# Optimization experiments

Hardware: AMD Instinct MI355X
Metric: run time of the kernel (lower is better)

Reference implementation:

```python
import jax, jax.numpy as jnp
import numpy as np

N, D, M, K = 65536, 128, 4096, 64

def _xavier_uniform(key, shape):
    fan_out, fan_in = shape
    limit = float(np.sqrt(6.0 / (fan_in + fan_out)))
    return jax.random.uniform(key, shape, jnp.float32, -limit, limit)

def setup_inputs() -> dict:
    key = jax.random.key(0)
    kx, ke, kd = jax.random.split(key, 3)
    x = jax.random.normal(kx, (N, D), jnp.float32)
    W_enc = _xavier_uniform(ke, (M, D))          # [n_latents, input_dim]
    W_dec = _xavier_uniform(kd, (D, M))          # [input_dim, n_latents]
    # normalize decoder columns to unit norm (dim=0), clamped at 1e-8
    norms = jnp.maximum(jnp.linalg.norm(W_dec, axis=0, keepdims=True), 1e-8)
    W_dec = W_dec / norms
    b_enc = jnp.zeros((M,), jnp.float32)
    b_dec = jnp.zeros((D,), jnp.float32)
    return {"x": x, "W_enc": W_enc, "b_enc": b_enc, "W_dec": W_dec, "b_dec": b_dec}

def reference(x, W_enc, b_enc, W_dec, b_dec):
    # encode: z_pre = relu(W_enc @ (x - b_dec) + b_enc)
    z_pre = jax.nn.relu((x - b_dec) @ W_enc.T + b_enc)          # [N, M]
    # TopK activation: keep k largest, zero the rest
    vals, idx = jax.lax.top_k(z_pre, K)                          # [N, K]
    rows = jnp.arange(z_pre.shape[0])[:, None]
    z = jnp.zeros_like(z_pre).at[rows, idx].set(vals)            # sparse [N, M]
    # decode: x_hat = z @ W_dec.T + b_dec
    x_hat = z @ W_dec.T + b_dec                                  # [N, D]
    return (x_hat, z)
```

## Files before the change

### kernel.cpp

```cpp
#include <hip/hip_runtime.h>
#include <cstdint>

#define DDIM 128
#define MLAT 4096
#define KSEL 64

typedef __bf16 bf16x8 __attribute__((ext_vector_type(8)));
typedef float  f32x4  __attribute__((ext_vector_type(4)));

__device__ __forceinline__ ushort bf16rn(float v) {
    unsigned b = __float_as_uint(v);
    return (ushort)((b + 0x7FFFu + ((b >> 16) & 1u)) >> 16);
}

__global__ __launch_bounds__(256) void k_prep(
        const float* __restrict__ x, const float* __restrict__ bdec,
        ushort* __restrict__ xhi, ushort* __restrict__ xlo,
        const float* __restrict__ Wenc,
        ushort* __restrict__ whiP, ushort* __restrict__ wloP,
        const float* __restrict__ Wdec, float* __restrict__ WdT) {
    int b = blockIdx.x;
    if (b < 8192) {
        int e = (b * 256 + threadIdx.x) * 4;
        float4 v = *(const float4*)(x + e);
        float4 bd = *(const float4*)(bdec + (e & 127));
        float a[4] = {v.x - bd.x, v.y - bd.y, v.z - bd.z, v.w - bd.w};
        ushort4 h, l;
        ushort* hp = (ushort*)&h; ushort* lp = (ushort*)&l;
#pragma unroll
        for (int i = 0; i < 4; ++i) {
            unsigned ua = __float_as_uint(a[i]);
            unsigned rh = (ua + 0x7FFFu + ((ua >> 16) & 1u)) & 0xFFFF0000u;
            float lo = a[i] - __uint_as_float(rh);
            hp[i] = (ushort)(rh >> 16);
            lp[i] = bf16rn(lo);
        }
        *(ushort4*)(xhi + e) = h;
        *(ushort4*)(xlo + e) = l;
    } else if (b < 8704) {
        int e = ((b - 8192) * 256 + threadIdx.x) * 4;
        float4 v = *(const float4*)(Wenc + e);
        float a[4] = {v.x, v.y, v.z, v.w};
        int c = e >> 7, k0 = e & 127;
        int ks = k0 >> 5, lq = (k0 >> 3) & 3, j0 = k0 & 7;
        int out = (((c >> 4) * 4 + ks) * 4 + lq) * 128 + (c & 15) * 8 + j0;
        ushort4 h, l;
        ushort* hp = (ushort*)&h; ushort* lp = (ushort*)&l;
#pragma unroll
        for (int i = 0; i < 4; ++i) {
            unsigned ua = __float_as_uint(a[i]);
            unsigned rh = (ua + 0x7FFFu + ((ua >> 16) & 1u)) & 0xFFFF0000u;
            float lo = a[i] - __uint_as_float(rh);
            hp[i] = (ushort)(rh >> 16);
            lp[i] = bf16rn(lo);
        }
        *(ushort4*)(whiP + out) = h;
        *(ushort4*)(wloP + out) = l;
    } else {
        int tid = (b - 8704) * 256 + threadIdx.x;
        int d = tid >> 12, j = tid & 4095;
        WdT[j * DDIM + d] = Wdec[tid];
    }
}

__global__ __launch_bounds__(256, 2) void k_encode_mfma(
        const ushort* __restrict__ xhi, const ushort* __restrict__ xlo,
        const ushort* __restrict__ whiP, const ushort* __restrict__ wloP,
        const float* __restrict__ benc, float* __restrict__ zout) {
    __shared__ __attribute__((aligned(16))) ushort Ah[128 * 128];
    __shared__ __attribute__((aligned(16))) ushort Al[128 * 128];

    const int t    = threadIdx.x;
    const int lane = t & 63;
    const int w    = t >> 6;
    const int i0   = blockIdx.x << 7;

    {
        int row = t >> 1, half = t & 1;
        const ushort* sh = xhi + (size_t)(i0 + row) * DDIM + half * 64;
        const ushort* sl = xlo + (size_t)(i0 + row) * DDIM + half * 64;
        int base = row * 256 + half * 128;
        int swz  = (row & 7) << 4;
#pragma unroll
        for (int j = 0; j < 8; ++j) {
            int off = (base + j * 16) ^ swz;
            *(bf16x8*)((char*)Ah + off) = *(const bf16x8*)(sh + j * 8);
            *(bf16x8*)((char*)Al + off) = *(const bf16x8*)(sl + j * 8);
        }
    }
    __syncthreads();

    const int lr = lane & 15;
    const int lq = lane >> 4;

    for (int cp = 0; cp < 16; ++cp) {
        const int jb = cp * 256 + (w << 6);
        const int tb = jb >> 4;
        f32x4 acc[8][4];
#pragma unroll
        for (int rf = 0; rf < 8; ++rf)
#pragma unroll
            for (int cf = 0; cf < 4; ++cf) acc[rf][cf] = (f32x4){0.f, 0.f, 0.f, 0.f};

#define BOFF(cf, ks) ((size_t)((((tb + (cf)) << 2) + (ks)) << 9) + (lane << 3))
        bf16x8 bhc[4], blc[4];
#pragma unroll
        for (int cf = 0; cf < 4; ++cf) {
            bhc[cf] = *(const bf16x8*)(whiP + BOFF(cf, 0));
            blc[cf] = *(const bf16x8*)(wloP + BOFF(cf, 0));
        }
#pragma unroll
        for (int ks = 0; ks < 4; ++ks) {
            bf16x8 bhn[4], bln[4];
            if (ks < 3) {
#pragma unroll
                for (int cf = 0; cf < 4; ++cf) {
                    bhn[cf] = *(const bf16x8*)(whiP + BOFF(cf, ks + 1));
                    bln[cf] = *(const bf16x8*)(wloP + BOFF(cf, ks + 1));
                }
            }
#pragma unroll
            for (int rf = 0; rf < 8; ++rf) {
                int row = rf * 16 + lr;
                int off = (row * 256 + ks * 64 + lq * 16) ^ ((row & 7) << 4);
                bf16x8 ah = *(const bf16x8*)((const char*)Ah + off);
                bf16x8 al = *(const bf16x8*)((const char*)Al + off);
#pragma unroll
                for (int cf = 0; cf < 4; ++cf) {
                    acc[rf][cf] = __builtin_amdgcn_mfma_f32_16x16x32_bf16(ah, bhc[cf], acc[rf][cf], 0, 0, 0);
                    acc[rf][cf] = __builtin_amdgcn_mfma_f32_16x16x32_bf16(ah, blc[cf], acc[rf][cf], 0, 0, 0);
                    acc[rf][cf] = __builtin_amdgcn_mfma_f32_16x16x32_bf16(al, bhc[cf], acc[rf][cf], 0, 0, 0);
                }
            }
            if (ks < 3) {
#pragma unroll
                for (int cf = 0; cf < 4; ++cf) { bhc[cf] = bhn[cf]; blc[cf] = bln[cf]; }
            }
        }
#undef BOFF
#pragma unroll
        for (int rf = 0; rf < 8; ++rf)
#pragma unroll
            for (int cf = 0; cf < 4; ++cf) {
                int col = jb + cf * 16 + lr;
                float be = benc[col];
#pragma unroll
                for (int r = 0; r < 4; ++r) {
                    int row = i0 + rf * 16 + lq * 4 + r;
                    zout[(size_t)row * MLAT + col] = fmaxf(acc[rf][cf][r] + be, 0.f);
                }
            }
    }
}

__global__ __launch_bounds__(128, 8) void k_topk_decode(
        float* __restrict__ zbuf, float* __restrict__ xhat,
        const float* __restrict__ WdT, const float* __restrict__ bdec,
        const float* __restrict__ x, const float* __restrict__ Wenc,
        const float* __restrict__ benc) {
    __shared__ float sval[KSEL];
    __shared__ int   sidx[KSEL];
    __shared__ float bval[128];
    __shared__ int   bidx[128];
    __shared__ unsigned char bselm[128];
    __shared__ unsigned scom[4];
    __shared__ int stot[2];

    const int tid  = threadIdx.x;
    const int lane = tid & 63;
    const int w    = tid >> 6;
    const size_t row = blockIdx.x;
    float* zr = zbuf + row * MLAT;
    const uint4* zu = (const uint4*)zr + (w << 9);

    uint4 u[8];
#pragma unroll
    for (int q = 0; q < 8; ++q) u[q] = zu[(q << 6) + lane];

    unsigned mx = 0u;
#pragma unroll
    for (int q = 0; q < 8; ++q)
        mx = max(mx, max(max(u[q].x, u[q].y), max(u[q].z, u[q].w)));
#pragma unroll
    for (int d = 32; d >= 1; d >>= 1) mx = max(mx, (unsigned)__shfl_xor((int)mx, d, 64));
    if (lane == 0) scom[w] = mx;
    __syncthreads();
    mx = max(scom[0], scom[1]);
    __syncthreads();

#define CNT_GE(T, OUTC)                                              \
    {                                                                \
        int _c = 0;                                                  \
        _Pragma("unroll")                                            \
        for (int q = 0; q < 8; ++q) {                                \
            _c += __popcll(__ballot(u[q].x >= (T)));                 \
            _c += __popcll(__ballot(u[q].y >= (T)));                 \
            _c += __popcll(__ballot(u[q].z >= (T)));                 \
            _c += __popcll(__ballot(u[q].w >= (T)));                 \
        }                                                            \
        if (lane == 0) scom[2 + w] = (unsigned)_c;                   \
        __syncthreads();                                             \
        OUTC = (int)(scom[2] + scom[3]);                             \
        __syncthreads();                                             \
    }

    unsigned T;
    {
        unsigned hi = mx + 1u;
        unsigned lo = (mx > 0x01800000u) ? (mx - 0x01800000u) : 0u;
        int c;
        CNT_GE(lo, c);
        if (c < KSEL) { lo = 0u; c = MLAT; }
        if (c == KSEL) {
            T = lo;
        } else {
            for (;;) {
                if (hi - lo <= 1u) { T = lo; break; }
                unsigned mid = lo + ((hi - lo) >> 1);
                int cm;
                CNT_GE(mid, cm);
                if (cm == KSEL) { T = mid; break; }
                if (cm > KSEL) lo = mid; else hi = mid;
            }
        }
    }

    const float tau   = __uint_as_float(T);
    const float DELTA = 2.5e-4f;
    const float PAD   = 5.0e-5f;
    const unsigned DH = __float_as_uint(tau + DELTA + PAD);
    const unsigned DL = __float_as_uint(fmaxf(tau - DELTA, 0.f));

    unsigned inm = 0u, bandm = 0u;
#pragma unroll
    for (int q = 0; q < 8; ++q) {
        unsigned vv[4] = {u[q].x, u[q].y, u[q].z, u[q].w};
#pragma unroll
        for (int c = 0; c < 4; ++c) {
            unsigned bit = 1u << (4 * q + c);
            if (vv[c] > DH) inm |= bit;
            else if (vv[c] >= DL) bandm |= bit;
        }
    }
    {
        int packed = (__popc(inm) << 16) | __popc(bandm);
#pragma unroll
        for (int d = 32; d >= 1; d >>= 1) packed += __shfl_xor(packed, d, 64);
        if (lane == 0) scom[2 + w] = (unsigned)packed;
        __syncthreads();
    }
    int A   = (int)((scom[2] >> 16) + (scom[3] >> 16));
    int BCt = (int)((scom[2] & 0xFFFFu) + (scom[3] & 0xFFFFu));
    __syncthreads();
    int need = KSEL - A;

    unsigned sel;
    if (need <= 0) {
        sel = inm;
    } else if (BCt == need) {
        sel = inm | bandm;
    } else {
        int BC2 = min(BCt, 128);
        int bc = __popc(bandm);
        int pre = bc;
#pragma unroll
        for (int d = 1; d < 64; d <<= 1) {
            int y = __shfl_up(pre, d, 64);
            if (lane >= d) pre += y;
        }
        int wtot = __shfl(pre, 63, 64);
        if (lane == 0) stot[w] = wtot;
        __syncthreads();
        int sbase = (pre - bc) + (w ? stot[0] : 0);
        {
            unsigned mm = bandm; int o = 0;
            while (mm) {
                int bp = __ffs(mm) - 1; mm &= mm - 1;
                int slot = sbase + o; ++o;
                if (slot < 128)
                    bidx[slot] = (w << 11) + ((bp >> 2) << 8) + (lane << 2) + (bp & 3);
            }
        }
        __syncthreads();
        for (int s = tid; s < BC2; s += 128) {
            int j = bidx[s];
            const float* wr = Wenc + (size_t)j * DDIM;
            const float* xr = x + row * DDIM;
            float a = 0.f;
            for (int k = 0; k < DDIM; ++k) a = fmaf(xr[k] - bdec[k], wr[k], a);
            bval[s] = fmaxf(a + benc[j], 0.f);
        }
        __syncthreads();
        if (tid == 0) {
            for (int s = 0; s < BC2; ++s) bselm[s] = 0;
            int take = min(need, BC2);
            for (int it = 0; it < take; ++it) {
                float bv = -1.f; int bi = 0x7FFFFFFF, bs = 0;
                for (int s = 0; s < BC2; ++s) {
                    if (bselm[s]) continue;
                    float v = bval[s]; int j = bidx[s];
                    if (v > bv || (v == bv && j < bi)) { bv = v; bi = j; bs = s; }
                }
                bselm[bs] = 1;
            }
        }
        __syncthreads();
        sel = inm;
        {
            unsigned mm = bandm; int o = 0;
            while (mm) {
                int bp = __ffs(mm) - 1; mm &= mm - 1;
                int slot = sbase + o; ++o;
                if (slot < 128 && bselm[slot]) sel |= 1u << bp;
            }
        }
        __syncthreads();
    }

    int scnt = __popc(sel);
    int pre = scnt;
#pragma unroll
    for (int d = 1; d < 64; d <<= 1) {
        int y = __shfl_up(pre, d, 64);
        if (lane >= d) pre += y;
    }
    int wtot2 = __shfl(pre, 63, 64);
    if (lane == 0) stot[w] = wtot2;
    __syncthreads();
    int pos = pre - scnt + (w ? stot[0] : 0);
    int total = stot[0] + stot[1];

    uint4* zw = (uint4*)zr + (w << 9);
#pragma unroll
    for (int q = 0; q < 8; ++q) {
        uint4 o;
        bool s0 = (sel >> (4 * q + 0)) & 1u;
        bool s1 = (sel >> (4 * q + 1)) & 1u;
        bool s2 = (sel >> (4 * q + 2)) & 1u;
        bool s3 = (sel >> (4 * q + 3)) & 1u;
        o.x = s0 ? u[q].x : 0u;
        o.y = s1 ? u[q].y : 0u;
        o.z = s2 ? u[q].z : 0u;
        o.w = s3 ? u[q].w : 0u;
        int base = (w << 11) + (q << 8) + (lane << 2);
        if (s0 && pos < KSEL) { sval[pos] = __uint_as_float(u[q].x); sidx[pos] = base + 0; ++pos; }
        if (s1 && pos < KSEL) { sval[pos] = __uint_as_float(u[q].y); sidx[pos] = base + 1; ++pos; }
        if (s2 && pos < KSEL) { sval[pos] = __uint_as_float(u[q].z); sidx[pos] = base + 2; ++pos; }
        if (s3 && pos < KSEL) { sval[pos] = __uint_as_float(u[q].w); sidx[pos] = base + 3; ++pos; }
        zw[(q << 6) + lane] = o;
    }
    __syncthreads();

    float a = bdec[tid];
    int tt = min(total, KSEL);
#pragma unroll 4
    for (int s = 0; s < tt; ++s) {
        float v = sval[s];
        int   j = sidx[s];
        a = fmaf(v, WdT[(size_t)j * DDIM + tid], a);
    }
    xhat[row * DDIM + tid] = a;
}

extern "C" void kernel_launch(void* const* d_in, const int* in_sizes, int n_in,
                              void* d_out, int out_size, void* d_ws, size_t ws_size,
                              hipStream_t stream) {
    const float* x    = (const float*)d_in[0];
    const float* Wenc = (const float*)d_in[1];
    const float* benc = (const float*)d_in[2];
    const float* Wdec = (const float*)d_in[3];
    const float* bdec = (const float*)d_in[4];

    const int N = in_sizes[0] / DDIM;
    float* xhat = (float*)d_out;
    float* zbuf = (float*)d_out + (size_t)N * DDIM;

    ushort* xhi = (ushort*)d_out;
    ushort* xlo = xhi + (size_t)N * DDIM;

    ushort* whiP = (ushort*)d_ws;
    ushort* wloP = whiP + (size_t)MLAT * DDIM;
    float*  WdT  = (float*)((char*)d_ws + 2u * 1024u * 1024u);

    k_prep<<<dim3(8192 + 512 + 2048), dim3(256), 0, stream>>>(
        x, bdec, xhi, xlo, Wenc, whiP, wloP, Wdec, WdT);
    k_encode_mfma<<<dim3(N / 128), dim3(256), 0, stream>>>(
        xhi, xlo, whiP, wloP, benc, zbuf);
    k_topk_decode<<<dim3(N), dim3(128), 0, stream>>>(
        zbuf, xhat, WdT, bdec, x, Wenc, benc);
}
```

Baseline: 842.8 us.

## Fuse x bf16 split into encode kernel, add nontemporal stores, drop barriers

Moves the x minus b_dec hi/lo bf16 split from the prep kernel into the encode kernel's shared-memory load. This removes the write and reread of the 64 MB xhi/xlo buffers. The z and x_hat stores and the z loads now use nontemporal builtins. Count reductions in the top-k kernel use double-buffered shared slots so one barrier per step can be dropped. The extra conversion work inside encode adds a little latency before the MFMA loop starts.

```diff
diff --git a/kernel.cpp b/kernel.cpp
--- a/kernel.cpp
+++ b/kernel.cpp
@@ -5,8 +5,10 @@
 #define MLAT 4096
 #define KSEL 64
 
-typedef __bf16 bf16x8 __attribute__((ext_vector_type(8)));
-typedef float  f32x4  __attribute__((ext_vector_type(4)));
+typedef __bf16  bf16x8  __attribute__((ext_vector_type(8)));
+typedef float   f32x4   __attribute__((ext_vector_type(4)));
+typedef ushort  ushort8 __attribute__((ext_vector_type(8)));
+typedef unsigned uint32x4 __attribute__((ext_vector_type(4)));
 
 __device__ __forceinline__ ushort bf16rn(float v) {
     unsigned b = __float_as_uint(v);
@@ -14,31 +16,12 @@
 }
 
 __global__ __launch_bounds__(256) void k_prep(
-        const float* __restrict__ x, const float* __restrict__ bdec,
-        ushort* __restrict__ xhi, ushort* __restrict__ xlo,
         const float* __restrict__ Wenc,
         ushort* __restrict__ whiP, ushort* __restrict__ wloP,
         const float* __restrict__ Wdec, float* __restrict__ WdT) {
     int b = blockIdx.x;
-    if (b < 8192) {
+    if (b < 512) {
         int e = (b * 256 + threadIdx.x) * 4;
-        float4 v = *(const float4*)(x + e);
-        float4 bd = *(const float4*)(bdec + (e & 127));
-        float a[4] = {v.x - bd.x, v.y - bd.y, v.z - bd.z, v.w - bd.w};
-        ushort4 h, l;
-        ushort* hp = (ushort*)&h; ushort* lp = (ushort*)&l;
-#pragma unroll
-        for (int i = 0; i < 4; ++i) {
-            unsigned ua = __float_as_uint(a[i]);
-            unsigned rh = (ua + 0x7FFFu + ((ua >> 16) & 1u)) & 0xFFFF0000u;
-            float lo = a[i] - __uint_as_float(rh);
-            hp[i] = (ushort)(rh >> 16);
-            lp[i] = bf16rn(lo);
-        }
-        *(ushort4*)(xhi + e) = h;
-        *(ushort4*)(xlo + e) = l;
-    } else if (b < 8704) {
-        int e = ((b - 8192) * 256 + threadIdx.x) * 4;
         float4 v = *(const float4*)(Wenc + e);
         float a[4] = {v.x, v.y, v.z, v.w};
         int c = e >> 7, k0 = e & 127;
@@ -57,14 +40,14 @@
         *(ushort4*)(whiP + out) = h;
         *(ushort4*)(wloP + out) = l;
     } else {
-        int tid = (b - 8704) * 256 + threadIdx.x;
+        int tid = (b - 512) * 256 + threadIdx.x;
         int d = tid >> 12, j = tid & 4095;
         WdT[j * DDIM + d] = Wdec[tid];
     }
 }
 
 __global__ __launch_bounds__(256, 2) void k_encode_mfma(
-        const ushort* __restrict__ xhi, const ushort* __restrict__ xlo,
+        const float* __restrict__ x, const float* __restrict__ bdec,
         const ushort* __restrict__ whiP, const ushort* __restrict__ wloP,
         const float* __restrict__ benc, float* __restrict__ zout) {
     __shared__ __attribute__((aligned(16))) ushort Ah[128 * 128];
@@ -77,15 +60,30 @@
 
     {
         int row = t >> 1, half = t & 1;
-        const ushort* sh = xhi + (size_t)(i0 + row) * DDIM + half * 64;
-        const ushort* sl = xlo + (size_t)(i0 + row) * DDIM + half * 64;
+        const float* xr = x + (size_t)(i0 + row) * DDIM + half * 64;
+        const float* bd = bdec + half * 64;
         int base = row * 256 + half * 128;
         int swz  = (row & 7) << 4;
 #pragma unroll
         for (int j = 0; j < 8; ++j) {
+            float4 v0 = *(const float4*)(xr + j * 8);
+            float4 v1 = *(const float4*)(xr + j * 8 + 4);
+            float4 b0 = *(const float4*)(bd + j * 8);
+            float4 b1 = *(const float4*)(bd + j * 8 + 4);
+            float a[8] = {v0.x - b0.x, v0.y - b0.y, v0.z - b0.z, v0.w - b0.w,
+                          v1.x - b1.x, v1.y - b1.y, v1.z - b1.z, v1.w - b1.w};
+            ushort8 h8, l8;
+#pragma unroll
+            for (int i = 0; i < 8; ++i) {
+                unsigned ua = __float_as_uint(a[i]);
+                unsigned rh = (ua + 0x7FFFu + ((ua >> 16) & 1u)) & 0xFFFF0000u;
+                float lo = a[i] - __uint_as_float(rh);
+                h8[i] = (ushort)(rh >> 16);
+                l8[i] = bf16rn(lo);
+            }
             int off = (base + j * 16) ^ swz;
-            *(bf16x8*)((char*)Ah + off) = *(const bf16x8*)(sh + j * 8);
-            *(bf16x8*)((char*)Al + off) = *(const bf16x8*)(sl + j * 8);
+            *(ushort8*)((char*)Ah + off) = h8;
+            *(ushort8*)((char*)Al + off) = l8;
         }
     }
     __syncthreads();
@@ -147,7 +145,8 @@
 #pragma unroll
                 for (int r = 0; r < 4; ++r) {
                     int row = i0 + rf * 16 + lq * 4 + r;
-                    zout[(size_t)row * MLAT + col] = fmaxf(acc[rf][cf][r] + be, 0.f);
+                    __builtin_nontemporal_store(fmaxf(acc[rf][cf][r] + be, 0.f),
+                                                &zout[(size_t)row * MLAT + col]);
                 }
             }
     }
@@ -163,7 +162,7 @@
     __shared__ float bval[128];
     __shared__ int   bidx[128];
     __shared__ unsigned char bselm[128];
-    __shared__ unsigned scom[4];
+    __shared__ unsigned scom[6];
     __shared__ int stot[2];
 
     const int tid  = threadIdx.x;
@@ -171,37 +170,37 @@
     const int w    = tid >> 6;
     const size_t row = blockIdx.x;
     float* zr = zbuf + row * MLAT;
-    const uint4* zu = (const uint4*)zr + (w << 9);
-
-    uint4 u[8];
-#pragma unroll
-    for (int q = 0; q < 8; ++q) u[q] = zu[(q << 6) + lane];
+    const uint32x4* zu = (const uint32x4*)zr + (w << 9);
+
+    uint32x4 u[8];
+#pragma unroll
+    for (int q = 0; q < 8; ++q) u[q] = __builtin_nontemporal_load(zu + (q << 6) + lane);
 
     unsigned mx = 0u;
 #pragma unroll
     for (int q = 0; q < 8; ++q)
-        mx = max(mx, max(max(u[q].x, u[q].y), max(u[q].z, u[q].w)));
+        mx = max(mx, max(max(u[q][0], u[q][1]), max(u[q][2], u[q][3])));
 #pragma unroll
     for (int d = 32; d >= 1; d >>= 1) mx = max(mx, (unsigned)__shfl_xor((int)mx, d, 64));
     if (lane == 0) scom[w] = mx;
     __syncthreads();
     mx = max(scom[0], scom[1]);
-    __syncthreads();
-
+
+    unsigned par = 0;
 #define CNT_GE(T, OUTC)                                              \
     {                                                                \
         int _c = 0;                                                  \
         _Pragma("unroll")                                            \
         for (int q = 0; q < 8; ++q) {                                \
-            _c += __popcll(__ballot(u[q].x >= (T)));                 \
-            _c += __popcll(__ballot(u[q].y >= (T)));                 \
-            _c += __popcll(__ballot(u[q].z >= (T)));                 \
-            _c += __popcll(__ballot(u[q].w >= (T)));                 \
+            _c += __popcll(__ballot(u[q][0] >= (T)));                \
+            _c += __popcll(__ballot(u[q][1] >= (T)));                \
+            _c += __popcll(__ballot(u[q][2] >= (T)));                \
+            _c += __popcll(__ballot(u[q][3] >= (T)));                \
         }                                                            \
-        if (lane == 0) scom[2 + w] = (unsigned)_c;                   \
+        if (lane == 0) scom[2 + 2 * par + w] = (unsigned)_c;         \
         __syncthreads();                                             \
-        OUTC = (int)(scom[2] + scom[3]);                             \
-        __syncthreads();                                             \
+        OUTC = (int)(scom[2 + 2 * par] + scom[3 + 2 * par]);         \
+        par ^= 1u;                                                   \
     }
 
     unsigned T;
@@ -234,24 +233,22 @@
     unsigned inm = 0u, bandm = 0u;
 #pragma unroll
     for (int q = 0; q < 8; ++q) {
-        unsigned vv[4] = {u[q].x, u[q].y, u[q].z, u[q].w};
 #pragma unroll
         for (int c = 0; c < 4; ++c) {
             unsigned bit = 1u << (4 * q + c);
-            if (vv[c] > DH) inm |= bit;
-            else if (vv[c] >= DL) bandm |= bit;
+            if (u[q][c] > DH) inm |= bit;
+            else if (u[q][c] >= DL) bandm |= bit;
         }
     }
     {
         int packed = (__popc(inm) << 16) | __popc(bandm);
 #pragma unroll
         for (int d = 32; d >= 1; d >>= 1) packed += __shfl_xor(packed, d, 64);
-        if (lane == 0) scom[2 + w] = (unsigned)packed;
-        __syncthreads();
-    }
-    int A   = (int)((scom[2] >> 16) + (scom[3] >> 16));
-    int BCt = (int)((scom[2] & 0xFFFFu) + (scom[3] & 0xFFFFu));
-    __syncthreads();
+        if (lane == 0) scom[2 + 2 * par + w] = (unsigned)packed;
+        __syncthreads();
+    }
+    int A   = (int)((scom[2 + 2 * par] >> 16) + (scom[3 + 2 * par] >> 16));
+    int BCt = (int)((scom[2 + 2 * par] & 0xFFFFu) + (scom[3 + 2 * par] & 0xFFFFu));
     int need = KSEL - A;
 
     unsigned sel;
@@ -330,24 +327,24 @@
     int pos = pre - scnt + (w ? stot[0] : 0);
     int total = stot[0] + stot[1];
 
-    uint4* zw = (uint4*)zr + (w << 9);
+    uint32x4* zw = (uint32x4*)zr + (w << 9);
 #pragma unroll
     for (int q = 0; q < 8; ++q) {
-        uint4 o;
+        uint32x4 o;
         bool s0 = (sel >> (4 * q + 0)) & 1u;
         bool s1 = (sel >> (4 * q + 1)) & 1u;
         bool s2 = (sel >> (4 * q + 2)) & 1u;
         bool s3 = (sel >> (4 * q + 3)) & 1u;
-        o.x = s0 ? u[q].x : 0u;
-        o.y = s1 ? u[q].y : 0u;
-        o.z = s2 ? u[q].z : 0u;
-        o.w = s3 ? u[q].w : 0u;
+        o[0] = s0 ? u[q][0] : 0u;
+        o[1] = s1 ? u[q][1] : 0u;
+        o[2] = s2 ? u[q][2] : 0u;
+        o[3] = s3 ? u[q][3] : 0u;
         int base = (w << 11) + (q << 8) + (lane << 2);
-        if (s0 && pos < KSEL) { sval[pos] = __uint_as_float(u[q].x); sidx[pos] = base + 0; ++pos; }
-        if (s1 && pos < KSEL) { sval[pos] = __uint_as_float(u[q].y); sidx[pos] = base + 1; ++pos; }
-        if (s2 && pos < KSEL) { sval[pos] = __uint_as_float(u[q].z); sidx[pos] = base + 2; ++pos; }
-        if (s3 && pos < KSEL) { sval[pos] = __uint_as_float(u[q].w); sidx[pos] = base + 3; ++pos; }
-        zw[(q << 6) + lane] = o;
+        if (s0 && pos < KSEL) { sval[pos] = __uint_as_float(u[q][0]); sidx[pos] = base + 0; ++pos; }
+        if (s1 && pos < KSEL) { sval[pos] = __uint_as_float(u[q][1]); sidx[pos] = base + 1; ++pos; }
+        if (s2 && pos < KSEL) { sval[pos] = __uint_as_float(u[q][2]); sidx[pos] = base + 2; ++pos; }
+        if (s3 && pos < KSEL) { sval[pos] = __uint_as_float(u[q][3]); sidx[pos] = base + 3; ++pos; }
+        __builtin_nontemporal_store(o, zw + (q << 6) + lane);
     }
     __syncthreads();
 
@@ -359,7 +356,7 @@
         int   j = sidx[s];
         a = fmaf(v, WdT[(size_t)j * DDIM + tid], a);
     }
-    xhat[row * DDIM + tid] = a;
+    __builtin_nontemporal_store(a, &xhat[row * DDIM + tid]);
 }
 
 extern "C" void kernel_launch(void* const* d_in, const int* in_sizes, int n_in,
@@ -375,17 +372,11 @@
     float* xhat = (float*)d_out;
     float* zbuf = (float*)d_out + (size_t)N * DDIM;
 
-    ushort* xhi = (ushort*)d_out;
-    ushort* xlo = xhi + (size_t)N * DDIM;
-
     ushort* whiP = (ushort*)d_ws;
     ushort* wloP = whiP + (size_t)MLAT * DDIM;
     float*  WdT  = (float*)((char*)d_ws + 2u * 1024u * 1024u);
 
-    k_prep<<<dim3(8192 + 512 + 2048), dim3(256), 0, stream>>>(
-        x, bdec, xhi, xlo, Wenc, whiP, wloP, Wdec, WdT);
-    k_encode_mfma<<<dim3(N / 128), dim3(256), 0, stream>>>(
-        xhi, xlo, whiP, wloP, benc, zbuf);
-    k_topk_decode<<<dim3(N), dim3(128), 0, stream>>>(
-        zbuf, xhat, WdT, bdec, x, Wenc, benc);
-}
+    k_prep<<<dim3(512 + 2048), dim3(256), 0, stream>>>(Wenc, whiP, wloP, Wdec, WdT);
+    k_encode_mfma<<<dim3(N / 128), dim3(256), 0, stream>>>(x, bdec, whiP, wloP, benc, zbuf);
+    k_topk_decode<<<dim3(N), dim3(128), 0, stream>>>(zbuf, xhat, WdT, bdec, x, Wenc, benc);
+}
```

New measurement: 900.5 us. 6.8% more time.
